# Kernel tuning notes

Measured on AMD Instinct MI355X. Metric: run time of the kernel, lower is better.

The kernel has to match this reference:

```python
import jax, jax.numpy as jnp
import numpy as np

STRIDE = 8
D_STATE = 16
D_CONV = 4
DT_RANK = 8
NB = 2            # mamba blocks per direction
B, F_IN, L_IN = 2, 256, 250
F_OUT = 128
KSIZE = 16
L_OUT = (L_IN - 1) * STRIDE + KSIZE   # 2008
D_INNER = 2 * F_OUT                   # 256
LN_EPS = 1e-5


def setup_inputs() -> dict:
    key = jax.random.key(0)
    ks = jax.random.split(key, 12)
    s = 0.05
    return {
        'x': jax.random.normal(ks[0], (B, F_IN, L_IN), jnp.float32),
        'skip': jax.random.normal(ks[1], (B, F_OUT, L_OUT), jnp.float32),
        'res_for': jnp.zeros((1,), jnp.float32),
        'res_back': jnp.zeros((1,), jnp.float32),
        'convT_w': jax.random.normal(ks[2], (F_IN, F_OUT, KSIZE), jnp.float32) * s,
        'convT_b': jnp.zeros((F_OUT,), jnp.float32),
        'fuse_w': jax.random.normal(ks[3], (F_OUT, 2 * F_OUT), jnp.float32) * s,
        'fuse_b': jnp.zeros((F_OUT,), jnp.float32),
        'norm_w': jnp.ones((2, NB, F_OUT), jnp.float32),
        'norm_b': jnp.zeros((2, NB, F_OUT), jnp.float32),
        'in_proj_w': jax.random.normal(ks[4], (2, NB, 2 * D_INNER, F_OUT), jnp.float32) * s,
        'conv_w': jax.random.normal(ks[5], (2, NB, D_INNER, 1, D_CONV), jnp.float32) * s,
        'conv_b': jnp.zeros((2, NB, D_INNER), jnp.float32),
        'x_proj_w': jax.random.normal(ks[6], (2, NB, DT_RANK + 2 * D_STATE, D_INNER), jnp.float32) * s,
        'dt_proj_w': jax.random.normal(ks[7], (2, NB, D_INNER, DT_RANK), jnp.float32) * s,
        'dt_proj_b': jax.random.uniform(ks[8], (2, NB, D_INNER), jnp.float32, -4.0, -2.0),
        'A_log': jnp.broadcast_to(jnp.log(jnp.arange(1, D_STATE + 1, dtype=jnp.float32)), (2, NB, D_INNER, D_STATE)) + jnp.zeros((2, NB, D_INNER, D_STATE), jnp.float32),
        'D_skip': jnp.ones((2, NB, D_INNER), jnp.float32),
        'out_proj_w': jax.random.normal(ks[9], (2, NB, F_OUT, D_INNER), jnp.float32) * s,
    }


def _layernorm(x, w, b):
    mu = x.mean(-1, keepdims=True)
    var = ((x - mu) ** 2).mean(-1, keepdims=True)
    return (x - mu) * jax.lax.rsqrt(var + LN_EPS) * w + b


def _mamba_mixer(x, p):
    # x: [B,L,D] -> [B,L,D]
    Bb, L, _ = x.shape
    xz = jnp.einsum('bld,ed->ble', x, p['in_proj_w'])          # [B,L,2*d_in]
    xc, z = xz[..., :D_INNER], xz[..., D_INNER:]
    # causal depthwise conv1d (pad left d_conv-1)
    conv = jax.lax.conv_general_dilated(
        xc.transpose(0, 2, 1), p['conv_w'], (1,), [(D_CONV - 1, 0)],
        feature_group_count=D_INNER, dimension_numbers=('NCH', 'OIH', 'NCH'))
    xc = jax.nn.silu(conv + p['conv_b'][None, :, None]).transpose(0, 2, 1)  # [B,L,d_in]
    xdbl = jnp.einsum('bld,ed->ble', xc, p['x_proj_w'])        # [B,L,dt_rank+2N]
    dt = xdbl[..., :DT_RANK]
    Bm = xdbl[..., DT_RANK:DT_RANK + D_STATE]                  # [B,L,N]
    Cm = xdbl[..., DT_RANK + D_STATE:]                         # [B,L,N]
    delta = jax.nn.softplus(jnp.einsum('blr,dr->bld', dt, p['dt_proj_w']) + p['dt_proj_b'])
    A = -jnp.exp(p['A_log'])                                   # [d_in,N]

    def step(h, inp):
        d_t, B_t, C_t, u_t = inp                               # [B,d_in],[B,N],[B,N],[B,d_in]
        dA = jnp.exp(d_t[..., None] * A)                       # [B,d_in,N]
        h = dA * h + (d_t * u_t)[..., None] * B_t[:, None, :]
        y = jnp.einsum('bdn,bn->bd', h, C_t)
        return h, y

    h0 = jnp.zeros((Bb, D_INNER, D_STATE), xc.dtype)
    _, ys = jax.lax.scan(step, h0, (delta.transpose(1, 0, 2), Bm.transpose(1, 0, 2),
                                    Cm.transpose(1, 0, 2), xc.transpose(1, 0, 2)))
    y = ys.transpose(1, 0, 2) + xc * p['D_skip']               # [B,L,d_in]
    y = y * jax.nn.silu(z)
    return jnp.einsum('bld,od->blo', y, p['out_proj_w'])


def _mamba_stack(xseq, params, d):
    # prenorm residual blocks, as in mamba_ssm Block (fused_add_norm=False, LayerNorm)
    residual = None
    for i in range(NB):
        p = {k: params[k][d, i] for k in ('norm_w', 'norm_b', 'in_proj_w', 'conv_w', 'conv_b',
                                          'x_proj_w', 'dt_proj_w', 'dt_proj_b', 'A_log', 'D_skip', 'out_proj_w')}
        residual = xseq if residual is None else xseq + residual
        xseq = _mamba_mixer(_layernorm(residual, p['norm_w'], p['norm_b']), p)
    return xseq + residual


def _conv_transpose1d(x, w, b, stride):
    # torch ConvTranspose1d: x [B,Cin,L], w [Cin,Cout,K]
    K = w.shape[-1]
    w_t = jnp.flip(w, -1).transpose(1, 0, 2)                   # [Cout,Cin,K]
    y = jax.lax.conv_general_dilated(x, w_t, (1,), [(K - 1, K - 1)],
                                     lhs_dilation=(stride,),
                                     dimension_numbers=('NCH', 'OIH', 'NCH'))
    return y + b[None, :, None]


def _forward(x, skip, convT_w, convT_b, fuse_w, fuse_b, params):
    h = jax.nn.silu(_conv_transpose1d(x, convT_w, convT_b, STRIDE))
    pad = skip.shape[2] - h.shape[2]
    if pad > 0:
        h = jnp.pad(h, ((0, 0), (0, 0), (0, pad)))
    h = jnp.concatenate([skip, h], axis=1)                     # [B,2*F_OUT,L]
    h = jax.nn.silu(jnp.einsum('bcl,oc->bol', h, fuse_w) + fuse_b[None, :, None])
    xs = h.transpose(0, 2, 1)                                  # [B,L,F_OUT]
    xf = _mamba_stack(xs, params, 0)
    xb = jnp.flip(_mamba_stack(jnp.flip(xs, 1), params, 1), 1)
    return (xf + xb).transpose(0, 2, 1)                        # [B,F_OUT,L]


def reference(x, skip, res_for, res_back, convT_w, convT_b, fuse_w, fuse_b,
              norm_w, norm_b, in_proj_w, conv_w, conv_b, x_proj_w,
              dt_proj_w, dt_proj_b, A_log, D_skip, out_proj_w):
    params = dict(norm_w=norm_w, norm_b=norm_b, in_proj_w=in_proj_w, conv_w=conv_w,
                  conv_b=conv_b, x_proj_w=x_proj_w, dt_proj_w=dt_proj_w, dt_proj_b=dt_proj_b,
                  A_log=A_log, D_skip=D_skip, out_proj_w=out_proj_w)
    return _forward(x, skip, convT_w, convT_b, fuse_w, fuse_b, params)
```

## Files before the change

kernel.cpp:

```cpp
#include <hip/hip_runtime.h>
#include <hip/hip_bf16.h>
#include <math.h>

#define B_    2
#define FIN_  256
#define LIN_  250
#define F_    128
#define K_    16
#define ST_   8
#define L_    2008
#define DI_   256
#define DS_   16
#define RK_   8
#define CV_   4
#define NBLK_ 2
#define NC_   64
#define CL_   32
#define RL_   ((size_t)B_ * L_)

__device__ __forceinline__ float silu_f(float x) {
    return x / (1.f + __expf(-x));
}
__device__ __forceinline__ float softplus_f(float x) {
    return (x > 20.f) ? x : log1pf(__expf(x));
}
__device__ __forceinline__ float dot4(float4 a, float4 b) {
    return a.x * b.x + a.y * b.y + a.z * b.z + a.w * b.w;
}

#define PREP_N (524288 + 32768 + 262144 + 262144 + 65536)
__global__ void prep_k(const float* __restrict__ convT_w, const float* __restrict__ fuse_w,
                       const float* __restrict__ in_proj, const float* __restrict__ out_proj,
                       const float* __restrict__ x_proj,
                       float* __restrict__ W2p, float* __restrict__ fwTp,
                       float* __restrict__ ipTp, float* __restrict__ opTp,
                       float* __restrict__ xpTp) {
    size_t g = (size_t)blockIdx.x * 256 + threadIdx.x;
    if (g >= PREP_N) return;
    if (g < 524288) {
        int ccq = g >> 12, rr = g & 4095;
        int po = rr >> 2, i = rr & 3;
        int cc = ccq * 4 + i;
        int p = po >> 7, o = po & 127;
        int c = cc & 255, k = (cc < 256) ? p : p + 8;
        W2p[g] = convT_w[(size_t)c * 2048 + o * 16 + k];
        return;
    }
    g -= 524288;
    if (g < 32768) {
        int cq = g >> 9, rr = g & 511;
        int o = rr >> 2, i = rr & 3;
        fwTp[g] = fuse_w[(size_t)o * 256 + cq * 4 + i];
        return;
    }
    g -= 32768;
    if (g < 262144) {
        int db = g >> 16, r = g & 65535;
        int cq = r >> 11, rr = r & 2047;
        int e = rr >> 2, i = rr & 3;
        ipTp[g] = in_proj[(size_t)db * 65536 + e * 128 + cq * 4 + i];
        return;
    }
    g -= 262144;
    if (g < 262144) {
        int db = g >> 15, r = g & 32767;
        int cq = r >> 9, rr = r & 511;
        int o = rr >> 2, i = rr & 3;
        opTp[g] = out_proj[(size_t)db * 32768 + o * 256 + cq * 4 + i];
        return;
    }
    g -= 262144;
    {
        int db = g >> 14, r = g & 16383;
        int cq = r >> 8, rr = r & 255;
        int e = rr >> 2, i = rr & 3;
        xpTp[g] = (e < 40) ? x_proj[(size_t)db * 10240 + e * 256 + cq * 4 + i] : 0.f;
    }
}

__global__ void __launch_bounds__(256) convt5_k(
        const float* __restrict__ x, const float* __restrict__ W2p,
        const float* __restrict__ bias, float* __restrict__ hT) {
    int j0 = blockIdx.x * 4, nt = blockIdx.y, b = blockIdx.z;
    int po = nt * 512 + threadIdx.x;
    int p = po >> 7, o = po & 127;

    __shared__ float xr[5][264];

    for (int idx = threadIdx.x; idx < 5 * 256; idx += 256) {
        int i = idx >> 8, c = idx & 255;
        int j = j0 - 1 + i;
        xr[i][c] = (j >= 0 && j < LIN_) ? x[((size_t)b * FIN_ + c) * LIN_ + j] : 0.f;
    }
    __syncthreads();

    float acca[4] = {0.f, 0.f, 0.f, 0.f};
    float accb[4] = {0.f, 0.f, 0.f, 0.f};
    const float4* W4 = (const float4*)W2p;

    for (int ccq = 0; ccq < 64; ++ccq) {
        float4 wa1 = W4[(size_t)ccq * 1024 + po];
        float4 wb1 = W4[(size_t)ccq * 1024 + po + 256];
        float4 wa2 = W4[(size_t)(ccq + 64) * 1024 + po];
        float4 wb2 = W4[(size_t)(ccq + 64) * 1024 + po + 256];
        float4 xv[5];
        #pragma unroll
        for (int i = 0; i < 5; ++i) xv[i] = *(const float4*)&xr[i][ccq * 4];
        #pragma unroll
        for (int jj = 0; jj < 4; ++jj) {
            acca[jj] += dot4(xv[jj + 1], wa1) + dot4(xv[jj], wa2);
            accb[jj] += dot4(xv[jj + 1], wb1) + dot4(xv[jj], wb2);
        }
    }
    float bo = bias[o];
    #pragma unroll
    for (int jj = 0; jj < 4; ++jj) {
        int j = j0 + jj;
        if (j <= 250) {
            hT[((size_t)b * L_ + 8 * j + p) * F_ + o]     = silu_f(acca[jj] + bo);
            hT[((size_t)b * L_ + 8 * j + p + 2) * F_ + o] = silu_f(accb[jj] + bo);
        }
    }
}

__global__ void __launch_bounds__(256) fuse5_k(
        const float* __restrict__ skip, const float* __restrict__ hT,
        const float* __restrict__ fwTp, const float* __restrict__ fb,
        float* __restrict__ xs) {
    int l0 = blockIdx.x * 8, b = blockIdx.y;
    int tid = threadIdx.x;

    __shared__ float ss[8][264];

    for (int idx = tid; idx < 128 * 8; idx += 256) {
        int c = idx >> 3, ll = idx & 7;
        ss[ll][c] = skip[((size_t)b * F_ + c) * L_ + l0 + ll];
    }
    for (int idx = tid; idx < 8 * 128; idx += 256) {
        int ll = idx >> 7, c = idx & 127;
        ss[ll][128 + c] = hT[((size_t)b * L_ + l0 + ll) * F_ + c];
    }
    __syncthreads();

    int o2 = tid & 63, rg = tid >> 6;
    float acca[2] = {0.f, 0.f}, accb[2] = {0.f, 0.f};
    const float4* W4 = (const float4*)fwTp;

    for (int cq = 0; cq < 64; ++cq) {
        float4 wa = W4[cq * 128 + o2];
        float4 wb = W4[cq * 128 + o2 + 64];
        #pragma unroll
        for (int rr = 0; rr < 2; ++rr) {
            float4 s = *(const float4*)&ss[rg * 2 + rr][cq * 4];
            acca[rr] += dot4(s, wa);
            accb[rr] += dot4(s, wb);
        }
    }
    float ba = fb[o2], bb = fb[o2 + 64];
    #pragma unroll
    for (int rr = 0; rr < 2; ++rr) {
        int l = l0 + rg * 2 + rr;
        float va = silu_f(acca[rr] + ba);
        float vb = silu_f(accb[rr] + bb);
        size_t rf = ((size_t)b * L_ + l) * F_;
        size_t rb = (RL_ + (size_t)b * L_ + (L_ - 1 - l)) * F_;
        xs[rf + o2] = va;       xs[rf + o2 + 64] = vb;
        xs[rb + o2] = va;       xs[rb + o2 + 64] = vb;
    }
}

__global__ void __launch_bounds__(256) ln5_k(
        const float* __restrict__ X, const float* __restrict__ nw,
        const float* __restrict__ nb_, const float* __restrict__ ipTp,
        float* __restrict__ XZ, int blk) {
    int rt = blockIdx.x, d = blockIdx.y;
    size_t rbase = (size_t)rt * 16;
    int tid = threadIdx.x, lane = tid & 63, wid = tid >> 6;
    int db = d * NBLK_ + blk;

    __shared__ float us[16][132];

    int wi0 = db * F_;
    #pragma unroll
    for (int rr = 0; rr < 4; ++rr) {
        int r = wid * 4 + rr;
        size_t row = rbase + r;
        float2 v = *(const float2*)(X + ((size_t)d * RL_ + row) * F_ + lane * 2);
        float s1 = v.x + v.y, s2 = v.x * v.x + v.y * v.y;
        for (int off = 32; off; off >>= 1) {
            s1 += __shfl_xor(s1, off);
            s2 += __shfl_xor(s2, off);
        }
        float mu = s1 * (1.f / F_);
        float var = s2 * (1.f / F_) - mu * mu;
        float rstd = rsqrtf(var + 1e-5f);
        int c = lane * 2;
        us[r][c]     = (v.x - mu) * rstd * nw[wi0 + c]     + nb_[wi0 + c];
        us[r][c + 1] = (v.y - mu) * rstd * nw[wi0 + c + 1] + nb_[wi0 + c + 1];
    }
    __syncthreads();

    int o = tid & 127, rh = tid >> 7;
    float acc0[8], acc1[8], acc2[8], acc3[8];
    #pragma unroll
    for (int i = 0; i < 8; ++i) { acc0[i] = acc1[i] = acc2[i] = acc3[i] = 0.f; }
    const float4* W4 = (const float4*)(ipTp + (size_t)db * 65536);

    for (int cq = 0; cq < 32; ++cq) {
        float4 w0 = W4[cq * 512 + o];
        float4 w1 = W4[cq * 512 + o + 128];
        float4 w2 = W4[cq * 512 + o + 256];
        float4 w3 = W4[cq * 512 + o + 384];
        #pragma unroll
        for (int rr = 0; rr < 8; ++rr) {
            float4 u = *(const float4*)&us[rh * 8 + rr][cq * 4];
            acc0[rr] += dot4(u, w0);
            acc1[rr] += dot4(u, w1);
            acc2[rr] += dot4(u, w2);
            acc3[rr] += dot4(u, w3);
        }
    }
    #pragma unroll
    for (int rr = 0; rr < 8; ++rr) {
        size_t row = rbase + rh * 8 + rr;
        float* dst = XZ + ((size_t)d * RL_ + row) * (2 * DI_);
        dst[o]       = acc0[rr];
        dst[o + 128] = acc1[rr];
        dst[o + 256] = acc2[rr];
        dst[o + 384] = acc3[rr];
    }
}

__global__ void __launch_bounds__(256) dwxdt_k(
        const float* __restrict__ XZ, const float* __restrict__ cw,
        const float* __restrict__ cb, const float* __restrict__ xpTp,
        const float* __restrict__ dtw, const float* __restrict__ dtb,
        float* __restrict__ XC, float* __restrict__ BCM,
        float* __restrict__ DELTA, int blk) {
    int rt = blockIdx.x, d = blockIdx.y;
    int tid = threadIdx.x;
    size_t rbase = (size_t)rt * 16;
    int db = d * NBLK_ + blk;

    __shared__ float xzs[19][264];
    __shared__ float xcs[16][264];
    __shared__ float dts[16][8];

    for (int idx = tid; idx < 19 * 256; idx += 256) {
        int s = idx >> 8;
        int c = idx & 255;
        long g = (long)rbase - 3 + s;
        xzs[s][c] = (g >= 0) ? XZ[((size_t)d * RL_ + g) * (2 * DI_) + c] : 0.f;
    }
    __syncthreads();

    {
        int ch = tid;
        int wi = db * DI_ + ch;
        float w0 = cw[(size_t)wi * CV_ + 0], w1 = cw[(size_t)wi * CV_ + 1];
        float w2 = cw[(size_t)wi * CV_ + 2], w3 = cw[(size_t)wi * CV_ + 3];
        float bias = cb[wi];
        #pragma unroll 4
        for (int r = 0; r < 16; ++r) {
            size_t row = rbase + r;
            int b = (row >= L_) ? 1 : 0;
            int l = (int)(row - (size_t)b * L_);
            int s = r + 3;
            float acc = bias + xzs[s][ch] * w3;
            if (l - 1 >= 0) acc += xzs[s - 1][ch] * w2;
            if (l - 2 >= 0) acc += xzs[s - 2][ch] * w1;
            if (l - 3 >= 0) acc += xzs[s - 3][ch] * w0;
            float v = silu_f(acc);
            xcs[r][ch] = v;
            XC[((size_t)d * RL_ + row) * DI_ + ch] = v;
        }
    }
    __syncthreads();

    {
        int e = tid & 63, rg = tid >> 6;
        float acc[4] = {0.f, 0.f, 0.f, 0.f};
        const float4* W4 = (const float4*)(xpTp + (size_t)db * 16384);
        for (int cq = 0; cq < 64; ++cq) {
            float4 w = W4[cq * 64 + e];
            #pragma unroll
            for (int rr = 0; rr < 4; ++rr)
                acc[rr] += dot4(*(const float4*)&xcs[rg * 4 + rr][cq * 4], w);
        }
        if (e < RK_) {
            #pragma unroll
            for (int rr = 0; rr < 4; ++rr) dts[rg * 4 + rr][e] = acc[rr];
        } else if (e < RK_ + 2 * DS_) {
            #pragma unroll
            for (int rr = 0; rr < 4; ++rr) {
                size_t row = rbase + rg * 4 + rr;
                BCM[((size_t)d * RL_ + row) * 32 + (e - RK_)] = acc[rr];
            }
        }
    }
    __syncthreads();

    {
        int ch = tid;
        int wi = db * DI_ + ch;
        float dwv[RK_];
        #pragma unroll
        for (int k = 0; k < RK_; ++k) dwv[k] = dtw[(size_t)wi * RK_ + k];
        float bias = dtb[wi];
        #pragma unroll 4
        for (int rr = 0; rr < 16; ++rr) {
            size_t row = rbase + rr;
            float acc = bias;
            #pragma unroll
            for (int k = 0; k < RK_; ++k) acc += dts[rr][k] * dwv[k];
            DELTA[((size_t)d * RL_ + row) * DI_ + ch] = softplus_f(acc);
        }
    }
}

__global__ void __launch_bounds__(256) scanA_k(
        float* __restrict__ DELTA, const float* __restrict__ XC,
        const float* __restrict__ BCM, const float* __restrict__ A_log,
        float* __restrict__ Y, float* __restrict__ hpart,
        float* __restrict__ dsum, int blk) {
    int d = blockIdx.z, cnk = blockIdx.y;
    int chunit0 = blockIdx.x * 16;
    int chl = threadIdx.x >> 4, n = threadIdx.x & 15;
    int b = chunit0 >> 8, ch0 = chunit0 & 255;
    int ch = ch0 + chl;
    int t0 = cnk * CL_;
    int nt = L_ - t0; if (nt > CL_) nt = CL_;

    __shared__ float dt_s[CL_][16];
    __shared__ float u_s[CL_][16];
    __shared__ float bc_s[CL_][32];

    size_t rowbase = (size_t)d * RL_ + (size_t)b * L_ + t0;
    for (int idx = threadIdx.x; idx < CL_ * 16; idx += 256) {
        int t = idx >> 4, c = idx & 15;
        float dv = 0.f, uv = 0.f;
        if (t < nt) {
            dv = DELTA[(rowbase + t) * DI_ + ch0 + c];
            uv = XC[(rowbase + t) * DI_ + ch0 + c];
        }
        dt_s[t][c] = dv; u_s[t][c] = uv;
    }
    for (int idx = threadIdx.x; idx < CL_ * 32; idx += 256) {
        int t = idx >> 5, m = idx & 31;
        bc_s[t][m] = (t < nt) ? BCM[(rowbase + t) * 32 + m] : 0.f;
    }
    __syncthreads();

    float A = -__expf(A_log[((size_t)(d * NBLK_ + blk) * DI_ + ch) * DS_ + n]);
    float h = 0.f, cum = 0.f;
    for (int t = 0; t < nt; ++t) {
        float dt = dt_s[t][chl];
        float u  = u_s[t][chl];
        float Bt = bc_s[t][n];
        float Ct = bc_s[t][16 + n];
        cum += dt;
        h = __expf(dt * A) * h + dt * u * Bt;
        float yp = h * Ct;
        yp += __shfl_xor(yp, 1);
        yp += __shfl_xor(yp, 2);
        yp += __shfl_xor(yp, 4);
        yp += __shfl_xor(yp, 8);
        if (n == 0) {
            Y[(rowbase + t) * DI_ + ch] = yp;
            DELTA[(rowbase + t) * DI_ + ch] = cum;
        }
    }
    size_t cb = (size_t)(d * B_ + b) * NC_ + cnk;
    hpart[cb * (DI_ * DS_) + ch * DS_ + n] = h;
    if (n == 0) dsum[cb * DI_ + ch] = cum;
}

__global__ void scanB_k(float* __restrict__ hpart, const float* __restrict__ dsum,
                        const float* __restrict__ A_log, int blk) {
    int d = blockIdx.y;
    int idx = blockIdx.x * 256 + threadIdx.x;
    int b = idx >> 12, ch = (idx >> 4) & 255, n = idx & 15;
    float A = -__expf(A_log[((size_t)(d * NBLK_ + blk) * DI_ + ch) * DS_ + n]);
    float h = 0.f;
    for (int c = 0; c < NC_; ++c) {
        size_t cb = (size_t)(d * B_ + b) * NC_ + c;
        size_t hi = cb * (DI_ * DS_) + ch * DS_ + n;
        float hc = hpart[hi];
        hpart[hi] = h;
        h = __expf(A * dsum[cb * DI_ + ch]) * h + hc;
    }
}

__global__ void __launch_bounds__(256) fixD_k(
        const float* __restrict__ DELTA , const float* __restrict__ BCM,
        const float* __restrict__ A_log, const float* __restrict__ hcarry,
        float* __restrict__ Y, int blk) {
    int d = blockIdx.z, cnk = blockIdx.y + 1;
    int chunit0 = blockIdx.x * 16;
    int b = chunit0 >> 8, ch0 = chunit0 & 255;
    int chl = threadIdx.x & 15, tg = threadIdx.x >> 4;
    int ch = ch0 + chl;
    int t0 = cnk * CL_;
    int nt = L_ - t0; if (nt > CL_) nt = CL_;

    __shared__ float cum_s[CL_][17];
    __shared__ float c_s[CL_][17];
    __shared__ float hin_s[16][16];

    size_t rowbase = (size_t)d * RL_ + (size_t)b * L_ + t0;
    for (int idx = threadIdx.x; idx < CL_ * 16; idx += 256) {
        int t = idx >> 4, c = idx & 15;
        float cv = 0.f, Cv = 0.f;
        if (t < nt) {
            cv = DELTA[(rowbase + t) * DI_ + ch0 + c];
            Cv = BCM[(rowbase + t) * 32 + 16 + c];
        }
        cum_s[t][c] = cv; c_s[t][c] = Cv;
    }
    {
        size_t cb = ((size_t)(d * B_ + b) * NC_ + cnk) * (DI_ * DS_);
        int cl = threadIdx.x >> 4, nn = threadIdx.x & 15;
        hin_s[cl][nn] = hcarry[cb + (ch0 + cl) * DS_ + nn];
    }
    __syncthreads();

    float An[16], Kn[16];
    const float* Ab = A_log + ((size_t)(d * NBLK_ + blk) * DI_ + ch) * DS_;
    #pragma unroll
    for (int n = 0; n < 16; ++n) {
        An[n] = -__expf(Ab[n]);
        Kn[n] = hin_s[chl][n];
    }
    #pragma unroll
    for (int tt = 0; tt < 2; ++tt) {
        int t = tg * 2 + tt;
        if (t < nt) {
            float cum = cum_s[t][chl];
            float corr = 0.f;
            #pragma unroll
            for (int n = 0; n < 16; ++n)
                corr += c_s[t][n] * Kn[n] * __expf(An[n] * cum);
            Y[(rowbase + t) * DI_ + ch] += corr;
        }
    }
}

__global__ void __launch_bounds__(256) gate5_k(
        const float* __restrict__ Y, const float* __restrict__ XC,
        const float* __restrict__ XZ, const float* __restrict__ Dsk,
        const float* __restrict__ opTp, const float* __restrict__ resid_in,
        float* __restrict__ outp, int blk) {
    int rt = blockIdx.x, d = blockIdx.y;
    int tid = threadIdx.x;
    size_t rbase = (size_t)rt * 16;
    int db = d * NBLK_ + blk;

    __shared__ float yg[16][264];

    {
        int c = tid;
        float Dc = Dsk[(size_t)db * DI_ + c];
        #pragma unroll 4
        for (int r = 0; r < 16; ++r) {
            size_t ri = (size_t)d * RL_ + rbase + r;
            float z = XZ[ri * (2 * DI_) + DI_ + c];
            yg[r][c] = (Y[ri * DI_ + c] + XC[ri * DI_ + c] * Dc) * silu_f(z);
        }
    }
    __syncthreads();

    int o2 = tid & 63, rg = tid >> 6;
    float acca[4] = {0.f, 0.f, 0.f, 0.f};
    float accb[4] = {0.f, 0.f, 0.f, 0.f};
    const float4* W4 = (const float4*)(opTp + (size_t)db * 32768);

    for (int cq = 0; cq < 64; ++cq) {
        float4 wa = W4[cq * 128 + o2];
        float4 wb = W4[cq * 128 + o2 + 64];
        #pragma unroll
        for (int rr = 0; rr < 4; ++rr) {
            float4 u = *(const float4*)&yg[rg * 4 + rr][cq * 4];
            acca[rr] += dot4(u, wa);
            accb[rr] += dot4(u, wb);
        }
    }
    #pragma unroll
    for (int rr = 0; rr < 4; ++rr) {
        size_t ri = (size_t)d * RL_ + rbase + rg * 4 + rr;
        float va = acca[rr], vb = accb[rr];
        if (resid_in) {
            va += resid_in[ri * F_ + o2];
            vb += resid_in[ri * F_ + o2 + 64];
        }
        outp[ri * F_ + o2]      = va;
        outp[ri * F_ + o2 + 64] = vb;
    }
}

__global__ void combine2_k(const float* __restrict__ cur, const float* __restrict__ res1,
                           float* __restrict__ out) {
    int l0 = blockIdx.x * 64, b = blockIdx.y;
    int tid = threadIdx.x;
    __shared__ float s[64][129];
    for (int idx = tid; idx < 64 * 128; idx += 256) {
        int ll = idx >> 7, o = idx & 127;
        int l = l0 + ll;
        if (l < L_) {
            size_t rf = ((size_t)b * L_ + l) * F_ + o;
            size_t rb = (RL_ + (size_t)b * L_ + (L_ - 1 - l)) * F_ + o;
            s[ll][o] = cur[rf] + res1[rf] + cur[rb] + res1[rb];
        }
    }
    __syncthreads();
    for (int idx = tid; idx < 64 * 128; idx += 256) {
        int o = idx >> 6, ll = idx & 63;
        int l = l0 + ll;
        if (l < L_) out[((size_t)b * F_ + o) * L_ + l] = s[ll][o];
    }
}

extern "C" void kernel_launch(void* const* d_in, const int* in_sizes, int n_in,
                              void* d_out, int out_size, void* d_ws, size_t ws_size,
                              hipStream_t stream) {
    const float* x        = (const float*)d_in[0];
    const float* skip     = (const float*)d_in[1];
    const float* convT_w  = (const float*)d_in[4];
    const float* convT_b  = (const float*)d_in[5];
    const float* fuse_w   = (const float*)d_in[6];
    const float* fuse_b   = (const float*)d_in[7];
    const float* norm_w   = (const float*)d_in[8];
    const float* norm_b   = (const float*)d_in[9];
    const float* in_proj  = (const float*)d_in[10];
    const float* conv_w   = (const float*)d_in[11];
    const float* conv_b   = (const float*)d_in[12];
    const float* x_proj   = (const float*)d_in[13];
    const float* dt_projw = (const float*)d_in[14];
    const float* dt_projb = (const float*)d_in[15];
    const float* A_log    = (const float*)d_in[16];
    const float* D_skip   = (const float*)d_in[17];
    const float* out_proj = (const float*)d_in[18];
    float* out = (float*)d_out;

    float* w = (float*)d_ws;
    size_t off = 0;
    auto alloc = [&](size_t n) { float* p = w + off; off += n; return p; };
    float* hT      = alloc((size_t)B_ * L_ * F_);
    float* W2p     = alloc(524288);
    float* fwTp    = alloc(32768);
    float* ipTp    = alloc(262144);
    float* opTp    = alloc(262144);
    float* xpTp    = alloc(65536);
    float* xs      = alloc(2 * RL_ * F_);
    float* cur     = alloc(2 * RL_ * F_);
    float* res1    = alloc(2 * RL_ * F_);
    float* xz      = alloc(2 * RL_ * (2 * DI_));
    float* xc      = alloc(2 * RL_ * DI_);
    float* dl      = alloc(2 * RL_ * DI_);
    float* bcm     = alloc(2 * RL_ * 32);
    float* yb      = alloc(2 * RL_ * DI_);
    float* hp   = hT;
    float* dsum = cur;
    (void)ws_size; (void)in_sizes; (void)n_in; (void)out_size;

    prep_k<<<(PREP_N + 255) / 256, 256, 0, stream>>>(convT_w, fuse_w, in_proj, out_proj,
                                                     x_proj, W2p, fwTp, ipTp, opTp, xpTp);
    convt5_k<<<dim3(63, 2, 2), 256, 0, stream>>>(x, W2p, convT_b, hT);
    fuse5_k<<<dim3(251, 2), 256, 0, stream>>>(skip, hT, fwTp, fuse_b, xs);

    for (int blk = 0; blk < NBLK_; ++blk) {
        const float* Xin = (blk == 0) ? xs : res1;
        ln5_k<<<dim3(251, 2), 256, 0, stream>>>(Xin, norm_w, norm_b, ipTp, xz, blk);
        dwxdt_k<<<dim3(251, 2), 256, 0, stream>>>(xz, conv_w, conv_b, xpTp,
                                                  dt_projw, dt_projb, xc, bcm, dl, blk);
        scanA_k<<<dim3(32, NC_, 2), 256, 0, stream>>>(dl, xc, bcm, A_log, yb, hp, dsum, blk);
        scanB_k<<<dim3(32, 2), 256, 0, stream>>>(hp, dsum, A_log, blk);
        fixD_k<<<dim3(32, NC_ - 1, 2), 256, 0, stream>>>(dl, bcm, A_log, hp, yb, blk);
        if (blk == 0)
            gate5_k<<<dim3(251, 2), 256, 0, stream>>>(yb, xc, xz, D_skip, opTp, xs, res1, 0);
        else
            gate5_k<<<dim3(251, 2), 256, 0, stream>>>(yb, xc, xz, D_skip, opTp, nullptr, cur, 1);
    }

    combine2_k<<<dim3(32, 2), 256, 0, stream>>>(cur, res1, out);
}
```

Measured before the change: 439.3 us.

## Fuse layernorm/in-proj with depthwise conv and fold chunk-carry correction into gate

Result: faster. 406.9 us (-7.4%).

```diff
diff --git a/kernel.cpp b/kernel.cpp
--- a/kernel.cpp
+++ b/kernel.cpp
@@ -169,23 +169,30 @@
     }
 }
 
-__global__ void __launch_bounds__(256) ln5_k(
+__global__ void __launch_bounds__(256) lndw_k(
         const float* __restrict__ X, const float* __restrict__ nw,
         const float* __restrict__ nb_, const float* __restrict__ ipTp,
-        float* __restrict__ XZ, int blk) {
+        const float* __restrict__ cw, const float* __restrict__ cb,
+        const float* __restrict__ xpTp, const float* __restrict__ dtw,
+        const float* __restrict__ dtb,
+        float* __restrict__ XC, float* __restrict__ XZz,
+        float* __restrict__ BCM, float* __restrict__ DELTA, int blk) {
     int rt = blockIdx.x, d = blockIdx.y;
     size_t rbase = (size_t)rt * 16;
     int tid = threadIdx.x, lane = tid & 63, wid = tid >> 6;
     int db = d * NBLK_ + blk;
-
-    __shared__ float us[16][132];
+    size_t dRL = (size_t)d * RL_;
+
+    __shared__ float us[19][132];
+    __shared__ float xcs[16][264];
+    __shared__ float dts[16][8];
 
     int wi0 = db * F_;
-    #pragma unroll
-    for (int rr = 0; rr < 4; ++rr) {
-        int r = wid * 4 + rr;
-        size_t row = rbase + r;
-        float2 v = *(const float2*)(X + ((size_t)d * RL_ + row) * F_ + lane * 2);
+    for (int r = wid; r < 19; r += 4) {
+        long grow = (long)rbase - 3 + r;
+        float2 v = make_float2(0.f, 0.f);
+        if (grow >= 0)
+            v = *(const float2*)(X + (dRL + (size_t)grow) * F_ + lane * 2);
         float s1 = v.x + v.y, s2 = v.x * v.x + v.y * v.y;
         for (int off = 32; off; off >>= 1) {
             s1 += __shfl_xor(s1, off);
@@ -194,115 +201,87 @@
         float mu = s1 * (1.f / F_);
         float var = s2 * (1.f / F_) - mu * mu;
         float rstd = rsqrtf(var + 1e-5f);
-        int c = lane * 2;
-        us[r][c]     = (v.x - mu) * rstd * nw[wi0 + c]     + nb_[wi0 + c];
-        us[r][c + 1] = (v.y - mu) * rstd * nw[wi0 + c + 1] + nb_[wi0 + c + 1];
-    }
-    __syncthreads();
-
-    int o = tid & 127, rh = tid >> 7;
-    float acc0[8], acc1[8], acc2[8], acc3[8];
+        int c2 = lane * 2;
+        us[r][c2]     = (v.x - mu) * rstd * nw[wi0 + c2]     + nb_[wi0 + c2];
+        us[r][c2 + 1] = (v.y - mu) * rstd * nw[wi0 + c2 + 1] + nb_[wi0 + c2 + 1];
+    }
+    __syncthreads();
+
+    int o = tid;
+    const float4* W4 = (const float4*)(ipTp + (size_t)db * 65536);
+
+    float acc[19];
     #pragma unroll
-    for (int i = 0; i < 8; ++i) { acc0[i] = acc1[i] = acc2[i] = acc3[i] = 0.f; }
-    const float4* W4 = (const float4*)(ipTp + (size_t)db * 65536);
-
+    for (int i = 0; i < 19; ++i) acc[i] = 0.f;
     for (int cq = 0; cq < 32; ++cq) {
-        float4 w0 = W4[cq * 512 + o];
-        float4 w1 = W4[cq * 512 + o + 128];
-        float4 w2 = W4[cq * 512 + o + 256];
-        float4 w3 = W4[cq * 512 + o + 384];
-        #pragma unroll
-        for (int rr = 0; rr < 8; ++rr) {
-            float4 u = *(const float4*)&us[rh * 8 + rr][cq * 4];
-            acc0[rr] += dot4(u, w0);
-            acc1[rr] += dot4(u, w1);
-            acc2[rr] += dot4(u, w2);
-            acc3[rr] += dot4(u, w3);
-        }
-    }
-    #pragma unroll
-    for (int rr = 0; rr < 8; ++rr) {
-        size_t row = rbase + rh * 8 + rr;
-        float* dst = XZ + ((size_t)d * RL_ + row) * (2 * DI_);
-        dst[o]       = acc0[rr];
-        dst[o + 128] = acc1[rr];
-        dst[o + 256] = acc2[rr];
-        dst[o + 384] = acc3[rr];
-    }
-}
-
-__global__ void __launch_bounds__(256) dwxdt_k(
-        const float* __restrict__ XZ, const float* __restrict__ cw,
-        const float* __restrict__ cb, const float* __restrict__ xpTp,
-        const float* __restrict__ dtw, const float* __restrict__ dtb,
-        float* __restrict__ XC, float* __restrict__ BCM,
-        float* __restrict__ DELTA, int blk) {
-    int rt = blockIdx.x, d = blockIdx.y;
-    int tid = threadIdx.x;
-    size_t rbase = (size_t)rt * 16;
-    int db = d * NBLK_ + blk;
-
-    __shared__ float xzs[19][264];
-    __shared__ float xcs[16][264];
-    __shared__ float dts[16][8];
-
-    for (int idx = tid; idx < 19 * 256; idx += 256) {
-        int s = idx >> 8;
-        int c = idx & 255;
-        long g = (long)rbase - 3 + s;
-        xzs[s][c] = (g >= 0) ? XZ[((size_t)d * RL_ + g) * (2 * DI_) + c] : 0.f;
-    }
-    __syncthreads();
-
-    {
-        int ch = tid;
-        int wi = db * DI_ + ch;
-        float w0 = cw[(size_t)wi * CV_ + 0], w1 = cw[(size_t)wi * CV_ + 1];
-        float w2 = cw[(size_t)wi * CV_ + 2], w3 = cw[(size_t)wi * CV_ + 3];
+        float4 w = W4[cq * 512 + o];
+        #pragma unroll
+        for (int r = 0; r < 19; ++r)
+            acc[r] += dot4(*(const float4*)&us[r][cq * 4], w);
+    }
+
+    {
+        int wi = db * DI_ + o;
+        float cw0 = cw[(size_t)wi * CV_ + 0], cw1 = cw[(size_t)wi * CV_ + 1];
+        float cw2 = cw[(size_t)wi * CV_ + 2], cw3 = cw[(size_t)wi * CV_ + 3];
         float bias = cb[wi];
-        #pragma unroll 4
-        for (int r = 0; r < 16; ++r) {
-            size_t row = rbase + r;
-            int b = (row >= L_) ? 1 : 0;
-            int l = (int)(row - (size_t)b * L_);
-            int s = r + 3;
-            float acc = bias + xzs[s][ch] * w3;
-            if (l - 1 >= 0) acc += xzs[s - 1][ch] * w2;
-            if (l - 2 >= 0) acc += xzs[s - 2][ch] * w1;
-            if (l - 3 >= 0) acc += xzs[s - 3][ch] * w0;
-            float v = silu_f(acc);
-            xcs[r][ch] = v;
-            XC[((size_t)d * RL_ + row) * DI_ + ch] = v;
-        }
+        #pragma unroll
+        for (int r16 = 0; r16 < 16; ++r16) {
+            size_t row = rbase + r16;
+            int b_r = (row >= L_) ? 1 : 0;
+            int l_r = (int)row - b_r * L_;
+            int s = r16 + 3;
+            float a = bias + acc[s] * cw3;
+            if (l_r - 1 >= 0) a += acc[s - 1] * cw2;
+            if (l_r - 2 >= 0) a += acc[s - 2] * cw1;
+            if (l_r - 3 >= 0) a += acc[s - 3] * cw0;
+            float v = silu_f(a);
+            xcs[r16][o] = v;
+            XC[(dRL + row) * DI_ + o] = v;
+        }
+    }
+
+    {
+        float accz[16];
+        #pragma unroll
+        for (int i = 0; i < 16; ++i) accz[i] = 0.f;
+        for (int cq = 0; cq < 32; ++cq) {
+            float4 w = W4[cq * 512 + 256 + o];
+            #pragma unroll
+            for (int r = 0; r < 16; ++r)
+                accz[r] += dot4(*(const float4*)&us[r + 3][cq * 4], w);
+        }
+        #pragma unroll
+        for (int r = 0; r < 16; ++r)
+            XZz[(dRL + rbase + r) * DI_ + o] = accz[r];
     }
     __syncthreads();
 
     {
         int e = tid & 63, rg = tid >> 6;
-        float acc[4] = {0.f, 0.f, 0.f, 0.f};
-        const float4* W4 = (const float4*)(xpTp + (size_t)db * 16384);
+        float acc2[4] = {0.f, 0.f, 0.f, 0.f};
+        const float4* Wx = (const float4*)(xpTp + (size_t)db * 16384);
         for (int cq = 0; cq < 64; ++cq) {
-            float4 w = W4[cq * 64 + e];
+            float4 w = Wx[cq * 64 + e];
             #pragma unroll
             for (int rr = 0; rr < 4; ++rr)
-                acc[rr] += dot4(*(const float4*)&xcs[rg * 4 + rr][cq * 4], w);
+                acc2[rr] += dot4(*(const float4*)&xcs[rg * 4 + rr][cq * 4], w);
         }
         if (e < RK_) {
             #pragma unroll
-            for (int rr = 0; rr < 4; ++rr) dts[rg * 4 + rr][e] = acc[rr];
+            for (int rr = 0; rr < 4; ++rr) dts[rg * 4 + rr][e] = acc2[rr];
         } else if (e < RK_ + 2 * DS_) {
             #pragma unroll
             for (int rr = 0; rr < 4; ++rr) {
                 size_t row = rbase + rg * 4 + rr;
-                BCM[((size_t)d * RL_ + row) * 32 + (e - RK_)] = acc[rr];
+                BCM[(dRL + row) * 32 + (e - RK_)] = acc2[rr];
             }
         }
     }
     __syncthreads();
 
     {
-        int ch = tid;
-        int wi = db * DI_ + ch;
+        int wi = db * DI_ + o;
         float dwv[RK_];
         #pragma unroll
         for (int k = 0; k < RK_; ++k) dwv[k] = dtw[(size_t)wi * RK_ + k];
@@ -310,10 +289,10 @@
         #pragma unroll 4
         for (int rr = 0; rr < 16; ++rr) {
             size_t row = rbase + rr;
-            float acc = bias;
+            float a = bias;
             #pragma unroll
-            for (int k = 0; k < RK_; ++k) acc += dts[rr][k] * dwv[k];
-            DELTA[((size_t)d * RL_ + row) * DI_ + ch] = softplus_f(acc);
+            for (int k = 0; k < RK_; ++k) a += dts[rr][k] * dwv[k];
+            DELTA[(dRL + row) * DI_ + o] = softplus_f(a);
         }
     }
 }
@@ -391,80 +370,74 @@
     }
 }
 
-__global__ void __launch_bounds__(256) fixD_k(
-        const float* __restrict__ DELTA , const float* __restrict__ BCM,
-        const float* __restrict__ A_log, const float* __restrict__ hcarry,
-        float* __restrict__ Y, int blk) {
-    int d = blockIdx.z, cnk = blockIdx.y + 1;
-    int chunit0 = blockIdx.x * 16;
-    int b = chunit0 >> 8, ch0 = chunit0 & 255;
-    int chl = threadIdx.x & 15, tg = threadIdx.x >> 4;
-    int ch = ch0 + chl;
-    int t0 = cnk * CL_;
-    int nt = L_ - t0; if (nt > CL_) nt = CL_;
-
-    __shared__ float cum_s[CL_][17];
-    __shared__ float c_s[CL_][17];
-    __shared__ float hin_s[16][16];
-
-    size_t rowbase = (size_t)d * RL_ + (size_t)b * L_ + t0;
-    for (int idx = threadIdx.x; idx < CL_ * 16; idx += 256) {
-        int t = idx >> 4, c = idx & 15;
-        float cv = 0.f, Cv = 0.f;
-        if (t < nt) {
-            cv = DELTA[(rowbase + t) * DI_ + ch0 + c];
-            Cv = BCM[(rowbase + t) * 32 + 16 + c];
-        }
-        cum_s[t][c] = cv; c_s[t][c] = Cv;
-    }
-    {
-        size_t cb = ((size_t)(d * B_ + b) * NC_ + cnk) * (DI_ * DS_);
-        int cl = threadIdx.x >> 4, nn = threadIdx.x & 15;
-        hin_s[cl][nn] = hcarry[cb + (ch0 + cl) * DS_ + nn];
-    }
-    __syncthreads();
-
-    float An[16], Kn[16];
-    const float* Ab = A_log + ((size_t)(d * NBLK_ + blk) * DI_ + ch) * DS_;
-    #pragma unroll
-    for (int n = 0; n < 16; ++n) {
-        An[n] = -__expf(Ab[n]);
-        Kn[n] = hin_s[chl][n];
-    }
-    #pragma unroll
-    for (int tt = 0; tt < 2; ++tt) {
-        int t = tg * 2 + tt;
-        if (t < nt) {
-            float cum = cum_s[t][chl];
-            float corr = 0.f;
-            #pragma unroll
-            for (int n = 0; n < 16; ++n)
-                corr += c_s[t][n] * Kn[n] * __expf(An[n] * cum);
-            Y[(rowbase + t) * DI_ + ch] += corr;
-        }
-    }
-}
-
-__global__ void __launch_bounds__(256) gate5_k(
+__global__ void __launch_bounds__(256) gateC_k(
         const float* __restrict__ Y, const float* __restrict__ XC,
-        const float* __restrict__ XZ, const float* __restrict__ Dsk,
+        const float* __restrict__ XZz, const float* __restrict__ DELTA ,
+        const float* __restrict__ BCM, const float* __restrict__ A_log,
+        const float* __restrict__ hcarry, const float* __restrict__ Dsk,
         const float* __restrict__ opTp, const float* __restrict__ resid_in,
         float* __restrict__ outp, int blk) {
     int rt = blockIdx.x, d = blockIdx.y;
     int tid = threadIdx.x;
     size_t rbase = (size_t)rt * 16;
     int db = d * NBLK_ + blk;
+    size_t dRL = (size_t)d * RL_;
 
     __shared__ float yg[16][264];
+    __shared__ float Cs[16][16];
+
+    {
+        int r = tid >> 4, n = tid & 15;
+        Cs[r][n] = BCM[(dRL + rbase + r) * 32 + 16 + n];
+    }
+    __syncthreads();
 
     {
         int c = tid;
         float Dc = Dsk[(size_t)db * DI_ + c];
-        #pragma unroll 4
+
+        float An[16];
+        const float* Ab = A_log + ((size_t)db * DI_ + c) * DS_;
+        #pragma unroll
+        for (int n = 0; n < 16; ++n) An[n] = -__expf(Ab[n]);
+
+        int b0 = (rbase >= L_) ? 1 : 0;
+        int l0 = (int)rbase - b0 * L_;
+        int ck0 = l0 >> 5;
+        int b1 = (rbase + 15 >= L_) ? 1 : 0;
+        int l1 = (int)(rbase + 15) - b1 * L_;
+        int ck1 = l1 >> 5;
+        const float* hp0 = hcarry + ((size_t)(d * B_ + b0) * NC_ + ck0) * (DI_ * DS_) + (size_t)c * DS_;
+        const float* hp1 = hcarry + ((size_t)(d * B_ + b1) * NC_ + ck1) * (DI_ * DS_) + (size_t)c * DS_;
+        float K0[16], K1[16];
+        #pragma unroll
+        for (int q = 0; q < 4; ++q) {
+            float4 v0 = *(const float4*)(hp0 + q * 4);
+            float4 v1 = *(const float4*)(hp1 + q * 4);
+            K0[4*q] = v0.x; K0[4*q+1] = v0.y; K0[4*q+2] = v0.z; K0[4*q+3] = v0.w;
+            K1[4*q] = v1.x; K1[4*q+1] = v1.y; K1[4*q+2] = v1.z; K1[4*q+3] = v1.w;
+        }
+
         for (int r = 0; r < 16; ++r) {
-            size_t ri = (size_t)d * RL_ + rbase + r;
-            float z = XZ[ri * (2 * DI_) + DI_ + c];
-            yg[r][c] = (Y[ri * DI_ + c] + XC[ri * DI_ + c] * Dc) * silu_f(z);
+            size_t row = rbase + r;
+            size_t ri = dRL + row;
+            int b_r = (row >= L_) ? 1 : 0;
+            int l_r = (int)row - b_r * L_;
+            int ck_r = l_r >> 5;
+            float cum = DELTA[ri * DI_ + c];
+            float corr = 0.f;
+            if (b_r == b0 && ck_r == ck0) {
+                #pragma unroll
+                for (int n = 0; n < 16; ++n)
+                    corr += Cs[r][n] * K0[n] * __expf(An[n] * cum);
+            } else {
+                #pragma unroll
+                for (int n = 0; n < 16; ++n)
+                    corr += Cs[r][n] * K1[n] * __expf(An[n] * cum);
+            }
+            float yv = Y[ri * DI_ + c] + corr;
+            float z  = XZz[ri * DI_ + c];
+            yg[r][c] = (yv + XC[ri * DI_ + c] * Dc) * silu_f(z);
         }
     }
     __syncthreads();
@@ -486,7 +459,7 @@
     }
     #pragma unroll
     for (int rr = 0; rr < 4; ++rr) {
-        size_t ri = (size_t)d * RL_ + rbase + rg * 4 + rr;
+        size_t ri = dRL + rbase + rg * 4 + rr;
         float va = acca[rr], vb = accb[rr];
         if (resid_in) {
             va += resid_in[ri * F_ + o2];
@@ -553,7 +526,7 @@
     float* xs      = alloc(2 * RL_ * F_);
     float* cur     = alloc(2 * RL_ * F_);
     float* res1    = alloc(2 * RL_ * F_);
-    float* xz      = alloc(2 * RL_ * (2 * DI_));
+    float* xzz     = alloc(2 * RL_ * DI_);
     float* xc      = alloc(2 * RL_ * DI_);
     float* dl      = alloc(2 * RL_ * DI_);
     float* bcm     = alloc(2 * RL_ * 32);
@@ -569,16 +542,18 @@
 
     for (int blk = 0; blk < NBLK_; ++blk) {
         const float* Xin = (blk == 0) ? xs : res1;
-        ln5_k<<<dim3(251, 2), 256, 0, stream>>>(Xin, norm_w, norm_b, ipTp, xz, blk);
-        dwxdt_k<<<dim3(251, 2), 256, 0, stream>>>(xz, conv_w, conv_b, xpTp,
-                                                  dt_projw, dt_projb, xc, bcm, dl, blk);
+        lndw_k<<<dim3(251, 2), 256, 0, stream>>>(Xin, norm_w, norm_b, ipTp,
+                                                 conv_w, conv_b, xpTp,
+                                                 dt_projw, dt_projb,
+                                                 xc, xzz, bcm, dl, blk);
         scanA_k<<<dim3(32, NC_, 2), 256, 0, stream>>>(dl, xc, bcm, A_log, yb, hp, dsum, blk);
         scanB_k<<<dim3(32, 2), 256, 0, stream>>>(hp, dsum, A_log, blk);
-        fixD_k<<<dim3(32, NC_ - 1, 2), 256, 0, stream>>>(dl, bcm, A_log, hp, yb, blk);
         if (blk == 0)
-            gate5_k<<<dim3(251, 2), 256, 0, stream>>>(yb, xc, xz, D_skip, opTp, xs, res1, 0);
+            gateC_k<<<dim3(251, 2), 256, 0, stream>>>(yb, xc, xzz, dl, bcm, A_log, hp,
+                                                      D_skip, opTp, xs, res1, 0);
         else
-            gate5_k<<<dim3(251, 2), 256, 0, stream>>>(yb, xc, xz, D_skip, opTp, nullptr, cur, 1);
+            gateC_k<<<dim3(251, 2), 256, 0, stream>>>(yb, xc, xzz, dl, bcm, A_log, hp,
+                                                      D_skip, opTp, nullptr, cur, 1);
     }
 
     combine2_k<<<dim3(32, 2), 256, 0, stream>>>(cur, res1, out);
```
